# Performance work log

Measured on AMD Instinct MI355X. Metric: run time of the kernel, lower is better.

Reference implementation:

```python
import jax, jax.numpy as jnp
import numpy as np

B, N, T = 64, 256, 512          # batch, num_objs, num_triples
DO, DP, H, DOUT = 512, 512, 512, 512


def setup_inputs() -> dict:
    key = jax.random.key(0)
    ks = jax.random.split(key, 12)

    def kaiming(k, shape):
        fan_in = shape[0]
        return jax.random.normal(k, shape, jnp.float32) * np.sqrt(2.0 / fan_in)

    return {
        "obj_vecs": jax.random.normal(ks[0], (B, N, DO), jnp.float32),
        "pred_vecs": jax.random.normal(ks[1], (B, T, DP), jnp.float32),
        "edges": jax.random.randint(ks[2], (B, T, 3), 0, N, jnp.int64),
        # net1: [2*DO+DP -> H -> 2*H+DOUT], ReLU after each Linear
        "n1_w1": kaiming(ks[3], (2 * DO + DP, H)),
        "n1_b1": jnp.zeros((H,), jnp.float32),
        "n1_w2": kaiming(ks[4], (H, 2 * H + DOUT)),
        "n1_b2": jnp.zeros((2 * H + DOUT,), jnp.float32),
        # net2: [H -> H -> DOUT], ReLU after each Linear
        "n2_w1": kaiming(ks[5], (H, H)),
        "n2_b1": jnp.zeros((H,), jnp.float32),
        "n2_w2": kaiming(ks[6], (H, DOUT)),
        "n2_b2": jnp.zeros((DOUT,), jnp.float32),
    }


def reference(obj_vecs, pred_vecs, edges,
              n1_w1, n1_b1, n1_w2, n1_b2,
              n2_w1, n2_b1, n2_w2, n2_b2):
    num_batch, num_objs, _ = obj_vecs.shape
    h_dim = n1_b1.shape[0]
    d_out = n2_w2.shape[1]

    s_idx = edges[:, :, 0]            # [B, T] subject node ids
    o_idx = edges[:, :, 2]            # [B, T] object node ids

    # gather subject/object vectors per triple
    cur_s = jnp.take_along_axis(obj_vecs, s_idx[:, :, None], axis=1)  # [B,T,DO]
    cur_o = jnp.take_along_axis(obj_vecs, o_idx[:, :, None], axis=1)  # [B,T,DO]
    cur_t = jnp.concatenate([cur_s, pred_vecs, cur_o], axis=-1)       # [B,T,2DO+DP]

    # net1 MLP (Linear+ReLU, Linear+ReLU)
    hid = jax.nn.relu(jnp.einsum('btd,dh->bth', cur_t, n1_w1) + n1_b1)
    new_t = jax.nn.relu(jnp.einsum('bth,hk->btk', hid, n1_w2) + n1_b2)

    new_s = new_t[:, :, :h_dim]
    new_p = new_t[:, :, h_dim:h_dim + d_out]
    new_o = new_t[:, :, h_dim + d_out:2 * h_dim + d_out]

    # scatter-add back to nodes, per batch element
    b_ix = jnp.arange(num_batch)[:, None]            # [B,1]
    pooled = jnp.zeros((num_batch, num_objs, h_dim), obj_vecs.dtype)
    pooled = pooled.at[b_ix, s_idx].add(new_s)
    pooled = pooled.at[b_ix, o_idx].add(new_o)

    # avg pooling: divide by per-node incidence count (clamped at 1)
    ones = jnp.ones(s_idx.shape, obj_vecs.dtype)
    counts = jnp.zeros((num_batch, num_objs), obj_vecs.dtype)
    counts = counts.at[b_ix, s_idx].add(ones)
    counts = counts.at[b_ix, o_idx].add(ones)
    counts = jnp.maximum(counts, 1.0)
    pooled = pooled / counts[:, :, None]

    # net2 MLP (Linear+ReLU, Linear+ReLU)
    h2 = jax.nn.relu(jnp.einsum('bnh,hk->bnk', pooled, n2_w1) + n2_b1)
    new_obj_vecs = jax.nn.relu(jnp.einsum('bnh,hd->bnd', h2, n2_w2) + n2_b2)

    return new_obj_vecs, new_p
```

## Files before the change

### kernel.cpp

```cpp
#include <hip/hip_runtime.h>

typedef __bf16 bf16;
typedef __attribute__((ext_vector_type(4))) __bf16 bf16x4;
typedef __attribute__((ext_vector_type(8))) __bf16 bf16x8;
typedef __attribute__((ext_vector_type(4))) float f32x4;

#define DEVINL __device__ __forceinline__

typedef __attribute__((address_space(1))) void gvoid_t;
typedef __attribute__((address_space(3))) void lvoid_t;

DEVINL void async_ld16(const void* g, void* l) {
    __builtin_amdgcn_global_load_lds((gvoid_t*)g, (lvoid_t*)l, 16, 0, 0);
}

template<int MODE>
__global__ __launch_bounds__(256, 2) void gemm_k(
    const bf16* __restrict__ A, const bf16* __restrict__ Bt,
    const float* __restrict__ bias, bf16* __restrict__ Dbf,
    float* __restrict__ Df, bf16* __restrict__ Dbf2,
    const int* __restrict__ edges, const bf16* __restrict__ obj,
    const bf16* __restrict__ pred, int K)
{
    const int tid = threadIdx.x;
    const int bm = blockIdx.x;
    const int bn = blockIdx.y;

    __shared__ __align__(16) bf16 ldsA[128 * 64];
    __shared__ __align__(16) bf16 ldsB[128 * 64];

    const int g_slot = tid & 7;
    const int row0 = tid >> 3;

    unsigned offS[4], offP[4], offO[4], offA[4], offB[4];
#pragma unroll
    for (int i = 0; i < 4; i++) {
        int r = row0 + 32 * i;
        int gr = bm * 128 + r;
        if (MODE == 0) {
            int b = gr >> 9;
            int s = edges[gr * 3 + 0] & 255;
            int o = edges[gr * 3 + 2] & 255;
            offS[i] = (unsigned)(b * 256 + s) * 512u;
            offP[i] = (unsigned)gr * 512u;
            offO[i] = (unsigned)(b * 256 + o) * 512u;
        } else {
            offA[i] = (unsigned)gr * (unsigned)K;
        }
        offB[i] = (unsigned)(bn * 128 + r) * (unsigned)K;
    }

    f32x4 acc[4][4];
    const f32x4 zero4 = {0.f, 0.f, 0.f, 0.f};
#pragma unroll
    for (int i = 0; i < 4; i++)
#pragma unroll
        for (int j = 0; j < 4; j++) acc[i][j] = zero4;

    const int wave = tid >> 6;
    const int lane = tid & 63;
    const int wr = (wave >> 1) * 64;
    const int wc = (wave & 1) * 64;
    const int lq = lane >> 4;
    const int lr = lane & 15;

    const int KT = K >> 6;
    for (int kt = 0; kt < KT; ++kt) {
        __syncthreads();
#pragma unroll
        for (int i = 0; i < 4; i++) {
            int r = row0 + 32 * i;
            int gsrc = g_slot ^ (r & 7);
            const bf16* gp;
            if (MODE == 0) {
                int region = kt >> 3;
                unsigned col = (unsigned)((kt & 7) * 64 + gsrc * 8);
                if (region == 0)      gp = obj + offS[i] + col;
                else if (region == 1) gp = pred + offP[i] + col;
                else                  gp = obj + offO[i] + col;
            } else {
                gp = A + offA[i] + (unsigned)(kt * 64 + gsrc * 8);
            }
            async_ld16(gp, ldsA + (tid + i * 256) * 8);
        }
#pragma unroll
        for (int i = 0; i < 4; i++) {
            int r = row0 + 32 * i;
            int gsrc = g_slot ^ (r & 7);
            async_ld16(Bt + offB[i] + (unsigned)(kt * 64 + gsrc * 8),
                       ldsB + (tid + i * 256) * 8);
        }
        __syncthreads();

#pragma unroll
        for (int ks = 0; ks < 2; ++ks) {
            bf16x8 af[4], bfr[4];
#pragma unroll
            for (int mi = 0; mi < 4; ++mi) {
                int r = wr + mi * 16 + lr;
                int g = (ks * 4 + lq) ^ (r & 7);
                af[mi] = *(const bf16x8*)(ldsA + (r * 8 + g) * 8);
            }
#pragma unroll
            for (int ni = 0; ni < 4; ++ni) {
                int r = wc + ni * 16 + lr;
                int g = (ks * 4 + lq) ^ (r & 7);
                bfr[ni] = *(const bf16x8*)(ldsB + (r * 8 + g) * 8);
            }
#pragma unroll
            for (int mi = 0; mi < 4; ++mi)
#pragma unroll
                for (int ni = 0; ni < 4; ++ni)
                    acc[mi][ni] = __builtin_amdgcn_mfma_f32_16x16x32_bf16(
                        af[mi], bfr[ni], acc[mi][ni], 0, 0, 0);
        }
    }

#pragma unroll
    for (int ni = 0; ni < 4; ++ni) {
        int col = bn * 128 + wc + ni * 16 + lr;
        float bv = bias[col];
#pragma unroll
        for (int mi = 0; mi < 4; ++mi) {
            int rowb = bm * 128 + wr + mi * 16 + lq * 4;
            f32x4 v = acc[mi][ni];
#pragma unroll
            for (int r = 0; r < 4; r++) {
                float x = v[r] + bv;
                x = x > 0.f ? x : 0.f;
                int grow = rowb + r;
                if (MODE == 1) {
                    if (col < 512)       Dbf[grow * 512 + col] = (bf16)x;
                    else if (col < 1024) Df[grow * 512 + (col - 512)] = x;
                    else                 Dbf2[grow * 512 + (col - 1024)] = (bf16)x;
                } else if (MODE == 3) {
                    Df[grow * 512 + col] = x;
                } else {
                    Dbf[grow * 512 + col] = (bf16)x;
                }
            }
        }
    }
}

__global__ void cvt_k(const float4* __restrict__ s, bf16x4* __restrict__ d) {
    int i = blockIdx.x * 256 + threadIdx.x;
    float4 v = s[i];
    bf16x4 o = { (bf16)v.x, (bf16)v.y, (bf16)v.z, (bf16)v.w };
    d[i] = o;
}

__global__ void transpose_k(const float* __restrict__ src, bf16* __restrict__ dst,
                            int R, int C) {
    __shared__ float tile[32][33];
    int c0 = blockIdx.x * 32, r0 = blockIdx.y * 32;
    int tx = threadIdx.x, ty = threadIdx.y;
#pragma unroll
    for (int i = 0; i < 4; i++)
        tile[ty + i * 8][tx] = src[(size_t)(r0 + ty + i * 8) * C + c0 + tx];
    __syncthreads();
#pragma unroll
    for (int i = 0; i < 4; i++)
        dst[(size_t)(c0 + ty + i * 8) * R + r0 + tx] = (bf16)tile[tx][ty + i * 8];
}

__global__ void zero_i4_k(int4* __restrict__ p) {
    p[blockIdx.x * 256 + threadIdx.x] = make_int4(0, 0, 0, 0);
}

__global__ void count_k(const int* __restrict__ edges, int* __restrict__ counts) {
    int e = blockIdx.x * 256 + threadIdx.x;
    int b = e >> 9;
    atomicAdd(counts + b * 256 + (edges[e * 3 + 0] & 255), 1);
    atomicAdd(counts + b * 256 + (edges[e * 3 + 2] & 255), 1);
}

__global__ void scan_k(const int* __restrict__ counts, int* __restrict__ starts,
                       int* __restrict__ cursor) {
    __shared__ int s[256];
    int b = blockIdx.x, t = threadIdx.x;
    int idx = b * 256 + t;
    int c0 = counts[idx];
    s[t] = c0;
    __syncthreads();
#pragma unroll
    for (int off = 1; off < 256; off <<= 1) {
        int v = (t >= off) ? s[t - off] : 0;
        __syncthreads();
        s[t] += v;
        __syncthreads();
    }
    int excl = b * 1024 + s[t] - c0;
    starts[idx] = excl;
    cursor[idx] = excl;
}

__global__ void fill_k(const int* __restrict__ edges, int* __restrict__ cursor,
                       int* __restrict__ entries) {
    int e = blockIdx.x * 256 + threadIdx.x;
    int b = e >> 9;
    int s = edges[e * 3 + 0] & 255;
    int o = edges[e * 3 + 2] & 255;
    int ps = atomicAdd(cursor + b * 256 + s, 1);
    entries[ps] = e << 1;
    int po = atomicAdd(cursor + b * 256 + o, 1);
    entries[po] = (e << 1) | 1;
}

__global__ void pool_k(const int* __restrict__ entries, const int* __restrict__ starts,
                       const int* __restrict__ counts,
                       const bf16* __restrict__ new_s, const bf16* __restrict__ new_o,
                       bf16* __restrict__ out) {
    __shared__ int ent[1024];
    int idx = blockIdx.x;
    int t = threadIdx.x;
    int c = counts[idx], st = starts[idx];
    for (int j = t; j < c; j += 256) ent[j] = entries[st + j];
    __syncthreads();
    float a0 = 0.f, a1 = 0.f;
    for (int j = 0; j < c; ++j) {
        int v = ent[j];
        const bf16* rp = ((v & 1) ? new_o : new_s) + (unsigned)(v >> 1) * 512u;
        a0 += (float)rp[t];
        a1 += (float)rp[t + 256];
    }
    float inv = 1.f / (float)(c > 1 ? c : 1);
    out[(unsigned)idx * 512u + t]       = (bf16)(a0 * inv);
    out[(unsigned)idx * 512u + t + 256] = (bf16)(a1 * inv);
}

extern "C" void kernel_launch(void* const* d_in, const int* in_sizes, int n_in,
                              void* d_out, int out_size, void* d_ws, size_t ws_size,
                              hipStream_t stream) {
    const float* obj_f  = (const float*)d_in[0];
    const float* pred_f = (const float*)d_in[1];
    const int*   edges  = (const int*)d_in[2];
    const float* w1 = (const float*)d_in[3];
    const float* b1 = (const float*)d_in[4];
    const float* w2 = (const float*)d_in[5];
    const float* b2 = (const float*)d_in[6];
    const float* w3 = (const float*)d_in[7];
    const float* b3 = (const float*)d_in[8];
    const float* w4 = (const float*)d_in[9];
    const float* b4 = (const float*)d_in[10];

    char* ws = (char*)d_ws;
    bf16* obj_bf  = (bf16*)(ws + 0);
    bf16* pred_bf = (bf16*)(ws + 16777216);
    bf16* new_s   = (bf16*)(ws + 0);
    int* entries  = (int*)(ws + 33554432);
    int* counts   = (int*)(ws + 33816576);
    int* starts   = (int*)(ws + 33882112);
    int* cursor   = (int*)(ws + 33947648);
    bf16* w1t = (bf16*)(ws + 50331648);
    bf16* w2t = (bf16*)(ws + 51904512);
    bf16* w3t = (bf16*)(ws + 53477376);
    bf16* w4t = (bf16*)(ws + 54001664);
    bf16* hid = (bf16*)(ws + 54525952);
    bf16* pooled_bf = hid;
    bf16* h2  = (bf16*)(ws + 71303168);

    float* out_obj = (float*)d_out;
    float* out_p   = (float*)d_out + 8388608;
    bf16* new_o    = (bf16*)d_out;

    cvt_k<<<8192, 256, 0, stream>>>((const float4*)obj_f, (bf16x4*)obj_bf);
    cvt_k<<<16384, 256, 0, stream>>>((const float4*)pred_f, (bf16x4*)pred_bf);
    transpose_k<<<dim3(16, 48), dim3(32, 8), 0, stream>>>(w1, w1t, 1536, 512);
    transpose_k<<<dim3(48, 16), dim3(32, 8), 0, stream>>>(w2, w2t, 512, 1536);
    transpose_k<<<dim3(16, 16), dim3(32, 8), 0, stream>>>(w3, w3t, 512, 512);
    transpose_k<<<dim3(16, 16), dim3(32, 8), 0, stream>>>(w4, w4t, 512, 512);

    gemm_k<0><<<dim3(256, 4), 256, 0, stream>>>(
        nullptr, w1t, b1, hid, nullptr, nullptr, edges, obj_bf, pred_bf, 1536);

    zero_i4_k<<<16, 256, 0, stream>>>((int4*)counts);
    count_k<<<128, 256, 0, stream>>>(edges, counts);
    scan_k<<<64, 256, 0, stream>>>(counts, starts, cursor);
    fill_k<<<128, 256, 0, stream>>>(edges, cursor, entries);

    gemm_k<1><<<dim3(256, 12), 256, 0, stream>>>(
        hid, w2t, b2, new_s, out_p, new_o, nullptr, nullptr, nullptr, 512);

    pool_k<<<16384, 256, 0, stream>>>(entries, starts, counts, new_s, new_o, pooled_bf);

    gemm_k<2><<<dim3(128, 4), 256, 0, stream>>>(
        pooled_bf, w3t, b3, h2, nullptr, nullptr, nullptr, nullptr, nullptr, 512);
    gemm_k<3><<<dim3(128, 4), 256, 0, stream>>>(
        h2, w4t, b4, nullptr, out_obj, nullptr, nullptr, nullptr, nullptr, 512);
}
```

Before: 428.2 us.

## Swap MFMA operands for row-contiguous vector stores and reorder block grid

Swaps the A and B operands of the MFMA so each lane ends up holding four consecutive output columns of a single row. The epilogue can then add bias with one vector load and write bf16x4 or f32x4 stores instead of scattered scalar stores. The grid is also transposed so consecutive blocks walk the N tiles of the same M tile, which should improve L2 reuse of the A rows (including the gathered rows in the first GEMM). The risk is mainly correctness of the transposed accumulator layout; the store width is still modest (8 or 16 bytes per lane).

```diff
diff --git a/kernel.cpp b/kernel.cpp
--- a/kernel.cpp
+++ b/kernel.cpp
@@ -23,8 +23,8 @@
     const bf16* __restrict__ pred, int K)
 {
     const int tid = threadIdx.x;
-    const int bm = blockIdx.x;
-    const int bn = blockIdx.y;
+    const int bn = blockIdx.x;
+    const int bm = blockIdx.y;
 
     __shared__ __align__(16) bf16 ldsA[128 * 64];
     __shared__ __align__(16) bf16 ldsB[128 * 64];
@@ -112,32 +112,39 @@
 #pragma unroll
                 for (int ni = 0; ni < 4; ++ni)
                     acc[mi][ni] = __builtin_amdgcn_mfma_f32_16x16x32_bf16(
-                        af[mi], bfr[ni], acc[mi][ni], 0, 0, 0);
+                        bfr[ni], af[mi], acc[mi][ni], 0, 0, 0);
         }
     }
 
 #pragma unroll
     for (int ni = 0; ni < 4; ++ni) {
-        int col = bn * 128 + wc + ni * 16 + lr;
-        float bv = bias[col];
+        int col = bn * 128 + wc + ni * 16 + lq * 4;
+        const f32x4 bv = *(const f32x4*)(bias + col);
 #pragma unroll
         for (int mi = 0; mi < 4; ++mi) {
-            int rowb = bm * 128 + wr + mi * 16 + lq * 4;
+            int row = bm * 128 + wr + mi * 16 + lr;
             f32x4 v = acc[mi][ni];
+            f32x4 x;
 #pragma unroll
             for (int r = 0; r < 4; r++) {
-                float x = v[r] + bv;
-                x = x > 0.f ? x : 0.f;
-                int grow = rowb + r;
-                if (MODE == 1) {
-                    if (col < 512)       Dbf[grow * 512 + col] = (bf16)x;
-                    else if (col < 1024) Df[grow * 512 + (col - 512)] = x;
-                    else                 Dbf2[grow * 512 + (col - 1024)] = (bf16)x;
-                } else if (MODE == 3) {
-                    Df[grow * 512 + col] = x;
+                float t = v[r] + bv[r];
+                x[r] = t > 0.f ? t : 0.f;
+            }
+            if (MODE == 1) {
+                if (col < 512) {
+                    bf16x4 o = { (bf16)x[0], (bf16)x[1], (bf16)x[2], (bf16)x[3] };
+                    *(bf16x4*)(Dbf + row * 512 + col) = o;
+                } else if (col < 1024) {
+                    *(f32x4*)(Df + row * 512 + (col - 512)) = x;
                 } else {
-                    Dbf[grow * 512 + col] = (bf16)x;
+                    bf16x4 o = { (bf16)x[0], (bf16)x[1], (bf16)x[2], (bf16)x[3] };
+                    *(bf16x4*)(Dbf2 + row * 512 + (col - 1024)) = o;
                 }
+            } else if (MODE == 3) {
+                *(f32x4*)(Df + row * 512 + col) = x;
+            } else {
+                bf16x4 o = { (bf16)x[0], (bf16)x[1], (bf16)x[2], (bf16)x[3] };
+                *(bf16x4*)(Dbf + row * 512 + col) = o;
             }
         }
     }
@@ -271,7 +278,7 @@
     transpose_k<<<dim3(16, 16), dim3(32, 8), 0, stream>>>(w3, w3t, 512, 512);
     transpose_k<<<dim3(16, 16), dim3(32, 8), 0, stream>>>(w4, w4t, 512, 512);
 
-    gemm_k<0><<<dim3(256, 4), 256, 0, stream>>>(
+    gemm_k<0><<<dim3(4, 256), 256, 0, stream>>>(
         nullptr, w1t, b1, hid, nullptr, nullptr, edges, obj_bf, pred_bf, 1536);
 
     zero_i4_k<<<16, 256, 0, stream>>>((int4*)counts);
@@ -279,13 +286,13 @@
     scan_k<<<64, 256, 0, stream>>>(counts, starts, cursor);
     fill_k<<<128, 256, 0, stream>>>(edges, cursor, entries);
 
-    gemm_k<1><<<dim3(256, 12), 256, 0, stream>>>(
+    gemm_k<1><<<dim3(12, 256), 256, 0, stream>>>(
         hid, w2t, b2, new_s, out_p, new_o, nullptr, nullptr, nullptr, 512);
 
     pool_k<<<16384, 256, 0, stream>>>(entries, starts, counts, new_s, new_o, pooled_bf);
 
-    gemm_k<2><<<dim3(128, 4), 256, 0, stream>>>(
+    gemm_k<2><<<dim3(4, 128), 256, 0, stream>>>(
         pooled_bf, w3t, b3, h2, nullptr, nullptr, nullptr, nullptr, nullptr, 512);
-    gemm_k<3><<<dim3(128, 4), 256, 0, stream>>>(
+    gemm_k<3><<<dim3(4, 128), 256, 0, stream>>>(
         h2, w4t, b4, nullptr, out_obj, nullptr, nullptr, nullptr, nullptr, 512);
 }
```

New measurement: 425.7 us. No clear change (-0.6%).
